# Optimization experiments

Hardware: AMD Instinct MI355X
Metric: run time of the kernel (lower is better)

## Reference

```python
import jax, jax.numpy as jnp
import numpy as np

B, S, D, H, F, L, V = 4, 512, 1024, 16, 4096, 6, 32000
HD = D // H
EPS = 1e-10


def layer_norm(x, g, b):
    m = x.mean(-1, keepdims=True)
    v = ((x - m) ** 2).mean(-1, keepdims=True)  # unbiased=False
    return g * (x - m) / jnp.sqrt(v + EPS) + b


def mha(q, k, v, wq, bq, wk, bk, wv, bv, wo, bo, mask):
    b_, s_, d_ = q.shape
    qh = (q @ wq + bq).reshape(b_, s_, H, HD).transpose(0, 2, 1, 3)  # [B,H,S,hd]
    kh = (k @ wk + bk).reshape(b_, s_, H, HD).transpose(0, 2, 1, 3)
    vh = (v @ wv + bv).reshape(b_, s_, H, HD).transpose(0, 2, 1, 3)
    score = jnp.einsum('bhqd,bhkd->bhqk', qh, kh) / jnp.sqrt(jnp.asarray(HD, q.dtype))
    score = jnp.where(mask == 0, jnp.asarray(-10000.0, q.dtype), score)
    attn = jax.nn.softmax(score, axis=-1)
    out = jnp.einsum('bhqk,bhkd->bhqd', attn, vh).transpose(0, 2, 1, 3).reshape(b_, s_, d_)
    return out @ wo + bo


def pos_encoding(seq, d):
    pos = jnp.arange(seq, dtype=jnp.float32)[:, None]
    i2 = jnp.arange(0, d, 2, dtype=jnp.float32)
    ang = pos / (10000.0 ** (i2 / d))
    enc = jnp.zeros((seq, d), jnp.float32)
    return enc.at[:, 0::2].set(jnp.sin(ang)).at[:, 1::2].set(jnp.cos(ang))


def setup_inputs() -> dict:
    key = jax.random.key(0)
    ks = iter(jax.random.split(key, 64))
    sd = 0.02
    inp = {
        'dec': jax.random.randint(next(ks), (B, S), 0, V),
        'enc': jax.random.normal(next(ks), (B, S, D), jnp.float32),
        't_mask': jnp.tril(jnp.ones((S, S), jnp.int32))[None, None],  # causal [1,1,S,S]
        's_mask': jnp.ones((1, 1, S, S), jnp.int32),
        'emb': (jax.random.normal(next(ks), (V, D), jnp.float32) * sd).at[1].set(0.0),  # padding_idx=1
    }
    for pre in ('sa', 'ca'):
        for nm in ('wq', 'wk', 'wv', 'wo'):
            inp[f'{pre}_{nm}'] = jax.random.normal(next(ks), (L, D, D), jnp.float32) * sd
            inp[f'{pre}_b{nm[1]}'] = jnp.zeros((L, D), jnp.float32)
    inp['ffn_w1'] = jax.random.normal(next(ks), (L, D, F), jnp.float32) * sd
    inp['ffn_b1'] = jnp.zeros((L, F), jnp.float32)
    inp['ffn_w2'] = jax.random.normal(next(ks), (L, F, D), jnp.float32) * sd
    inp['ffn_b2'] = jnp.zeros((L, D), jnp.float32)
    for i in (1, 2, 3):
        inp[f'ln{i}_g'] = jnp.ones((L, D), jnp.float32)
        inp[f'ln{i}_b'] = jnp.zeros((L, D), jnp.float32)
    inp['w_out'] = jax.random.normal(next(ks), (D, V), jnp.float32) * sd
    inp['b_out'] = jnp.zeros((V,), jnp.float32)
    return inp


def reference(dec, enc, t_mask, s_mask, emb,
              sa_wq, sa_bq, sa_wk, sa_bk, sa_wv, sa_bv, sa_wo, sa_bo,
              ca_wq, ca_bq, ca_wk, ca_bk, ca_wv, ca_bv, ca_wo, ca_bo,
              ffn_w1, ffn_b1, ffn_w2, ffn_b2,
              ln1_g, ln1_b, ln2_g, ln2_b, ln3_g, ln3_b, w_out, b_out):
    x = emb[dec] + pos_encoding(dec.shape[1], D)  # token + positional embedding
    for l in range(L):
        r = x
        a = mha(x, x, x, sa_wq[l], sa_bq[l], sa_wk[l], sa_bk[l], sa_wv[l], sa_bv[l], sa_wo[l], sa_bo[l], t_mask)
        x = layer_norm(a + r, ln1_g[l], ln1_b[l])
        r = x
        a = mha(x, enc, enc, ca_wq[l], ca_bq[l], ca_wk[l], ca_bk[l], ca_wv[l], ca_bv[l], ca_wo[l], ca_bo[l], s_mask)
        x = layer_norm(a + r, ln2_g[l], ln2_b[l])
        r = x
        f = jax.nn.relu(x @ ffn_w1[l] + ffn_b1[l]) @ ffn_w2[l] + ffn_b2[l]
        x = layer_norm(f + r, ln3_g[l], ln3_b[l])
    return x @ w_out + b_out  # [B,S,V] logits
```

## Files before the change

### kernel.cpp

```cpp
#include <hip/hip_runtime.h>
#include <hip/hip_bf16.h>
#include <math.h>

using bf16 = __hip_bfloat16;
typedef __attribute__((ext_vector_type(8))) short short8;
typedef __attribute__((ext_vector_type(4))) float f32x4;
typedef __attribute__((ext_vector_type(16))) float f32x16;

#define NTOKC 2048
#define DM 1024
#define SEQL 512
#define NHEADS 16
#define HDIM 64
#define FFDIM 4096
#define NLAYERS 6
#define VOCAB 32000

__device__ __forceinline__ void gld_lds16(const void* g, void* l) {
  __builtin_amdgcn_global_load_lds((__attribute__((address_space(1))) void*)g,
                                   (__attribute__((address_space(3))) void*)l, 16, 0, 0);
}

template<int BM, int BN>
__global__ __launch_bounds__(256, 3) void gemm_k(
    const bf16* __restrict__ A, const bf16* __restrict__ B, void* __restrict__ Cp,
    const float* __restrict__ bias, int K, int lda, int ldb, int ldc,
    long long sAb, long long sAh, long long sBb, long long sBh,
    long long sCb, long long sCh, int HH, int biasStride, float scale, int flags,
    int mTiles, const bf16* __restrict__ A2, int a2from)
{
  constexpr int WAM = BM/64;
  constexpr int WAN = 4/WAM;
  constexpr int WN  = BN/WAN;
  constexpr int FM  = 2;
  constexpr int FN  = WN/32;
  constexpr int NCA = (BM*64)/2048;
  constexpr int NCB = (BN*64)/2048;
  __shared__ __align__(16) bf16 As[BM*64];
  __shared__ __align__(16) bf16 Bs[BN*64];
  const int tid = threadIdx.x, w = tid>>6, l = tid&63;
  const int z = blockIdx.z, zb = z/HH, zh = z - zb*HH;
  const bf16* Abase = (zh >= a2from) ? A2 : A;
  const bf16* Ab = Abase + (size_t)zb*sAb + (size_t)zh*sAh;
  const bf16* Bb = B + (size_t)zb*sBb + (size_t)zh*sBh;

  const int nwg = gridDim.x;
  int o = blockIdx.x, idx = o;
  if ((nwg & 7) == 0) idx = (o & 7) * (nwg >> 3) + (o >> 3);
  const int mt = idx % mTiles, nt = idx / mTiles;
  const int m0 = mt*BM, n0 = nt*BN;

  const int wm = w / WAN, wn = w % WAN;
  const int lr = l & 31;
  const int lh = l >> 5;

  f32x16 acc[FM][FN];
  #pragma unroll
  for (int i=0;i<FM;i++)
    #pragma unroll
    for (int j=0;j<FN;j++)
      #pragma unroll
      for (int e=0;e<16;e++) acc[i][j][e] = 0.f;

  int rA[NCA], kA[NCA];
  #pragma unroll
  for (int c=0;c<NCA;c++){ int e=c*2048+tid*8; int r=e>>6, k=e&63; rA[c]=r; kA[c]=k ^ ((r&7)<<3); }
  int rB[NCB], kB[NCB];
  #pragma unroll
  for (int c=0;c<NCB;c++){ int e=c*2048+tid*8; int r=e>>6, k=e&63; rB[c]=r; kB[c]=k ^ ((r&7)<<3); }

  for (int kt=0; kt<K; kt+=64) {
    #pragma unroll
    for (int c=0;c<NCA;c++)
      gld_lds16(Ab + (size_t)(m0+rA[c])*lda + kt + kA[c], (char*)As + c*4096 + w*1024);
    #pragma unroll
    for (int c=0;c<NCB;c++)
      gld_lds16(Bb + (size_t)(n0+rB[c])*ldb + kt + kB[c], (char*)Bs + c*4096 + w*1024);
    __syncthreads();
    #pragma unroll
    for (int kq=0; kq<4; kq++) {
      const int kk = kq*16 + lh*8;
      short8 a_[FM], b_[FN];
      #pragma unroll
      for (int i=0;i<FM;i++) {
        const int row = wm*64 + i*32 + lr;
        a_[i] = *(const short8*)(As + row*64 + (kk ^ ((row&7)<<3)));
      }
      #pragma unroll
      for (int j=0;j<FN;j++) {
        const int row = wn*WN + j*32 + lr;
        b_[j] = *(const short8*)(Bs + row*64 + (kk ^ ((row&7)<<3)));
      }
      #pragma unroll
      for (int i=0;i<FM;i++)
        #pragma unroll
        for (int j=0;j<FN;j++)
          acc[i][j] = __builtin_amdgcn_mfma_f32_32x32x16_bf16(a_[i], b_[j], acc[i][j], 0,0,0);
    }
    __syncthreads();
  }

  const bool obf = flags & 1, orl = flags & 2;
  const size_t coff = (size_t)zb*sCb + (size_t)zh*sCh;
  const float* brow = bias ? (bias + (size_t)z*biasStride) : nullptr;
  #pragma unroll
  for (int i=0;i<FM;i++) {
    #pragma unroll
    for (int j=0;j<FN;j++) {
      const int col = n0 + wn*WN + j*32 + lr;
      const float bv = brow ? brow[col] : 0.f;
      const int row0 = m0 + wm*64 + i*32 + 4*lh;
      #pragma unroll
      for (int r=0;r<16;r++) {
        const int row = row0 + (r&3) + 8*(r>>2);
        float v = acc[i][j][r]*scale + bv;
        if (orl) v = fmaxf(v, 0.f);
        const size_t off = coff + (size_t)row*ldc + col;
        if (obf) ((bf16*)Cp)[off] = __float2bfloat16(v);
        else     ((float*)Cp)[off] = v;
      }
    }
  }
}

template<int CAUSAL>
__global__ __launch_bounds__(256, 4) void flash_k(
    const bf16* __restrict__ Qg, const bf16* __restrict__ Kg,
    const bf16* __restrict__ Vt, bf16* __restrict__ Og)
{
  constexpr int PADK = 72;
  __shared__ __align__(16) bf16 Ks[64*PADK];
  __shared__ __align__(16) bf16 Vs[64*PADK];
  __shared__ __align__(16) bf16 Ps[4*16*PADK];
  const int tid = threadIdx.x, w = tid>>6, l = tid&63;
  const int qt = blockIdx.x, bh = blockIdx.y;
  const int b = bh>>4, h = bh&15;
  const int q0 = qt*64;
  const int lr = l&15, lg = l>>4;

  const bf16* qrow = Qg + (size_t)(b*SEQL + q0 + w*16 + lr)*DM + h*HDIM + lg*8;
  short8 qf0 = *(const short8*)(qrow);
  short8 qf1 = *(const short8*)(qrow + 32);

  const f32x4 vzero = {0.f,0.f,0.f,0.f};
  f32x4 Oa[4];
  float mrow[4], lrow[4];
  #pragma unroll
  for (int j=0;j<4;j++) Oa[j] = vzero;
  #pragma unroll
  for (int r=0;r<4;r++){ mrow[r] = -INFINITY; lrow[r] = 0.f; }

  const int ntiles = CAUSAL ? (qt+1) : (SEQL/64);
  const int c0 = tid, c1 = tid + 256;
  const int r0_ = c0>>3, o0_ = (c0&7)*8, r1_ = c1>>3, o1_ = (c1&7)*8;

  short8 s0,s1,s2,s3;
  {
    s0 = *(const short8*)(Kg + (size_t)(b*SEQL + r0_)*DM + h*HDIM + o0_);
    s1 = *(const short8*)(Kg + (size_t)(b*SEQL + r1_)*DM + h*HDIM + o1_);
    s2 = *(const short8*)(Vt + ((size_t)bh*HDIM + r0_)*SEQL + o0_);
    s3 = *(const short8*)(Vt + ((size_t)bh*HDIM + r1_)*SEQL + o1_);
  }

  for (int t=0; t<ntiles; ++t) {
    __syncthreads();
    *(short8*)(Ks + r0_*PADK + o0_) = s0;
    *(short8*)(Ks + r1_*PADK + o1_) = s1;
    *(short8*)(Vs + r0_*PADK + o0_) = s2;
    *(short8*)(Vs + r1_*PADK + o1_) = s3;
    __syncthreads();
    if (t+1 < ntiles) {
      const int kv1 = (t+1)*64;
      s0 = *(const short8*)(Kg + (size_t)(b*SEQL + kv1 + r0_)*DM + h*HDIM + o0_);
      s1 = *(const short8*)(Kg + (size_t)(b*SEQL + kv1 + r1_)*DM + h*HDIM + o1_);
      s2 = *(const short8*)(Vt + ((size_t)bh*HDIM + r0_)*SEQL + kv1 + o0_);
      s3 = *(const short8*)(Vt + ((size_t)bh*HDIM + r1_)*SEQL + kv1 + o1_);
    }

    f32x4 sa[4];
    #pragma unroll
    for (int jg=0;jg<4;jg++) {
      short8 kb0 = *(const short8*)(Ks + (jg*16+lr)*PADK + lg*8);
      short8 kb1 = *(const short8*)(Ks + (jg*16+lr)*PADK + 32 + lg*8);
      sa[jg] = __builtin_amdgcn_mfma_f32_16x16x32_bf16(qf0, kb0, vzero, 0,0,0);
      sa[jg] = __builtin_amdgcn_mfma_f32_16x16x32_bf16(qf1, kb1, sa[jg], 0,0,0);
    }

    float pv[4][4];
    #pragma unroll
    for (int jg=0;jg<4;jg++)
      #pragma unroll
      for (int r=0;r<4;r++) {
        float sv = sa[jg][r]*0.125f;
        if (CAUSAL && t==ntiles-1) {
          if (jg*16+lr > w*16+lg*4+r) sv = -INFINITY;
        }
        pv[jg][r] = sv;
      }
    float tm[4], sf[4], rs[4];
    #pragma unroll
    for (int r=0;r<4;r++) {
      float mx = fmaxf(fmaxf(pv[0][r],pv[1][r]), fmaxf(pv[2][r],pv[3][r]));
      #pragma unroll
      for (int o=1;o<16;o<<=1) mx = fmaxf(mx, __shfl_xor(mx, o));
      tm[r] = fmaxf(mrow[r], mx);
      sf[r] = __expf(mrow[r]-tm[r]);
      mrow[r] = tm[r];
    }
    #pragma unroll
    for (int r=0;r<4;r++) {
      float acc = 0.f;
      #pragma unroll
      for (int jg=0;jg<4;jg++) { float e = __expf(pv[jg][r]-tm[r]); pv[jg][r]=e; acc += e; }
      #pragma unroll
      for (int o=1;o<16;o<<=1) acc += __shfl_xor(acc, o);
      rs[r] = acc;
      lrow[r] = lrow[r]*sf[r] + rs[r];
    }
    #pragma unroll
    for (int jg=0;jg<4;jg++)
      #pragma unroll
      for (int r=0;r<4;r++) Oa[jg][r] *= sf[r];

    bf16* pw = Ps + w*16*PADK;
    #pragma unroll
    for (int jg=0;jg<4;jg++)
      #pragma unroll
      for (int r=0;r<4;r++)
        pw[(lg*4+r)*PADK + jg*16+lr] = __float2bfloat16(pv[jg][r]);
    asm volatile("s_waitcnt lgkmcnt(0)" ::: "memory");
    __builtin_amdgcn_sched_barrier(0);
    short8 pa0 = *(const short8*)(pw + lr*PADK + lg*8);
    short8 pa1 = *(const short8*)(pw + lr*PADK + 32 + lg*8);
    #pragma unroll
    for (int jg=0;jg<4;jg++) {
      short8 vb0 = *(const short8*)(Vs + (jg*16+lr)*PADK + lg*8);
      short8 vb1 = *(const short8*)(Vs + (jg*16+lr)*PADK + 32 + lg*8);
      Oa[jg] = __builtin_amdgcn_mfma_f32_16x16x32_bf16(pa0, vb0, Oa[jg], 0,0,0);
      Oa[jg] = __builtin_amdgcn_mfma_f32_16x16x32_bf16(pa1, vb1, Oa[jg], 0,0,0);
    }
  }

  #pragma unroll
  for (int r=0;r<4;r++) {
    const float inv = 1.f/lrow[r];
    const size_t rb = (size_t)(b*SEQL + q0 + w*16 + lg*4 + r)*DM + h*HDIM;
    #pragma unroll
    for (int jg=0;jg<4;jg++)
      Og[rb + jg*16 + lr] = __float2bfloat16(Oa[jg][r]*inv);
  }
}

__global__ __launch_bounds__(256) void embed_k(const int* __restrict__ dec, const float* __restrict__ emb,
    float* __restrict__ x32, bf16* __restrict__ x16)
{
  const int idx = blockIdx.x*256 + threadIdx.x;
  const int d = idx & (DM-1), tok = idx >> 10, s = tok & (SEQL-1);
  const float e = emb[(size_t)dec[tok]*DM + d];
  const float den = powf(10000.f, (float)(d & ~1) * (1.f/(float)DM));
  const float ang = (float)s / den;
  const float pe = (d&1) ? cosf(ang) : sinf(ang);
  const float vv = e + pe;
  x32[idx] = vv; x16[idx] = __float2bfloat16(vv);
}

__global__ __launch_bounds__(256) void cvt_k(const float* __restrict__ in, bf16* __restrict__ out, int n){
  int i = blockIdx.x*256 + threadIdx.x;
  if (i < n) out[i] = __float2bfloat16(in[i]);
}

__global__ __launch_bounds__(256) void trans_k(const float* __restrict__ src, bf16* __restrict__ dst, int K, int N)
{
  __shared__ float t[32][33];
  const int n0 = blockIdx.x*32, k0 = blockIdx.y*32;
  const int tx = threadIdx.x&31, ty = threadIdx.x>>5;
  #pragma unroll
  for (int i=0;i<4;i++) t[ty+i*8][tx] = src[(size_t)(k0+ty+i*8)*N + n0+tx];
  __syncthreads();
  #pragma unroll
  for (int i=0;i<4;i++) dst[(size_t)(n0+ty+i*8)*K + k0+tx] = __float2bfloat16(t[tx][ty+i*8]);
}

struct TPack { const float* src[10]; bf16* dst[10]; int K[10]; int N[10]; int tile0[10]; };
__global__ __launch_bounds__(256) void transm_k(TPack p)
{
  __shared__ float t[32][33];
  const int id = blockIdx.x;
  int mi = 0;
  #pragma unroll
  for (int i=1;i<10;i++) if (id >= p.tile0[i]) mi = i;
  const float* src = p.src[mi]; bf16* dst = p.dst[mi];
  const int K = p.K[mi], N = p.N[mi];
  const int local = id - p.tile0[mi];
  const int ntn = N >> 5;
  const int nt = local % ntn, kt = local / ntn;
  const int n0 = nt*32, k0 = kt*32;
  const int tx = threadIdx.x&31, ty = threadIdx.x>>5;
  #pragma unroll
  for (int i=0;i<4;i++) t[ty+i*8][tx] = src[(size_t)(k0+ty+i*8)*N + n0+tx];
  __syncthreads();
  #pragma unroll
  for (int i=0;i<4;i++) dst[(size_t)(n0+ty+i*8)*K + k0+tx] = __float2bfloat16(t[tx][ty+i*8]);
}

struct BiasSrc { const float* s[6]; float* out; };
__global__ __launch_bounds__(256) void biaspack_k(BiasSrc p)
{
  const int i = blockIdx.x*256 + threadIdx.x;
  const int l = i / 6144, j = i - l*6144;
  const int m = j >> 10, c = j & 1023;
  p.out[i] = p.s[m][(size_t)l*DM + c];
}

__global__ __launch_bounds__(256) void vtrans_k(const bf16* __restrict__ v, bf16* __restrict__ vt)
{
  __shared__ bf16 t[32][33];
  const int bh = blockIdx.z, b = bh>>4, h = bh&15;
  const int s0 = blockIdx.x*32, d0 = blockIdx.y*32;
  const int tx = threadIdx.x&31, ty = threadIdx.x>>5;
  #pragma unroll
  for (int i=0;i<4;i++)
    t[ty+i*8][tx] = v[(size_t)(b*SEQL + s0+ty+i*8)*DM + h*HDIM + d0+tx];
  __syncthreads();
  #pragma unroll
  for (int i=0;i<4;i++)
    vt[((size_t)bh*HDIM + d0+ty+i*8)*SEQL + s0+tx] = t[tx][ty+i*8];
}

__global__ __launch_bounds__(256) void ln_k(const float* __restrict__ a, const float* __restrict__ r,
    const float* __restrict__ g, const float* __restrict__ be,
    float* __restrict__ y32, bf16* __restrict__ y16)
{
  const int row = blockIdx.x, t = threadIdx.x;
  const size_t base = (size_t)row*DM;
  float v[4]; float s = 0.f;
  #pragma unroll
  for (int i=0;i<4;i++){ int c=t+i*256; v[i] = a[base+c] + r[base+c]; s += v[i]; }
  __shared__ float red[8];
  #pragma unroll
  for (int o=32;o>0;o>>=1) s += __shfl_down(s,o);
  if ((t&63)==0) red[t>>6]=s;
  __syncthreads();
  const float mean = (red[0]+red[1]+red[2]+red[3]) * (1.f/1024.f);
  float vs = 0.f;
  #pragma unroll
  for (int i=0;i<4;i++){ float d=v[i]-mean; vs += d*d; }
  #pragma unroll
  for (int o=32;o>0;o>>=1) vs += __shfl_down(vs,o);
  if ((t&63)==0) red[4+(t>>6)]=vs;
  __syncthreads();
  const float var = (red[4]+red[5]+red[6]+red[7]) * (1.f/1024.f);
  const float rstd = rsqrtf(var + 1e-10f);
  #pragma unroll
  for (int i=0;i<4;i++){
    int c=t+i*256;
    float y = g[c]*(v[i]-mean)*rstd + be[c];
    y32[base+c] = y; y16[base+c] = __float2bfloat16(y);
  }
}

template<int CAUSAL>
static void run_attention(hipStream_t st, bf16* qkv, bf16* vt, bf16* ctx)
{
  vtrans_k<<<dim3(16,2,64),256,0,st>>>(qkv + (size_t)2*NTOKC*DM, vt);
  flash_k<CAUSAL><<<dim3(SEQL/64, 64),256,0,st>>>(qkv, qkv + (size_t)NTOKC*DM, vt, ctx);
}

extern "C" void kernel_launch(void* const* d_in, const int* in_sizes, int n_in,
                              void* d_out, int out_size, void* d_ws, size_t ws_size,
                              hipStream_t stream)
{
  (void)in_sizes; (void)n_in; (void)out_size;
  const int*   dec    = (const int*)  d_in[0];
  const float* enc    = (const float*)d_in[1];
  const float* emb    = (const float*)d_in[4];
  const float* sa_w[4] = { (const float*)d_in[5], (const float*)d_in[7], (const float*)d_in[9],  (const float*)d_in[11] };
  const float* sa_b[4] = { (const float*)d_in[6], (const float*)d_in[8], (const float*)d_in[10], (const float*)d_in[12] };
  const float* ca_w[4] = { (const float*)d_in[13], (const float*)d_in[15], (const float*)d_in[17], (const float*)d_in[19] };
  const float* ca_b[4] = { (const float*)d_in[14], (const float*)d_in[16], (const float*)d_in[18], (const float*)d_in[20] };
  const float* ffn_w1 = (const float*)d_in[21];
  const float* ffn_b1 = (const float*)d_in[22];
  const float* ffn_w2 = (const float*)d_in[23];
  const float* ffn_b2 = (const float*)d_in[24];
  const float* ln_g[3] = { (const float*)d_in[25], (const float*)d_in[27], (const float*)d_in[29] };
  const float* ln_b[3] = { (const float*)d_in[26], (const float*)d_in[28], (const float*)d_in[30] };
  const float* w_out  = (const float*)d_in[31];
  const float* b_out  = (const float*)d_in[32];
  float* out = (float*)d_out;

  char* p = (char*)d_ws;
  auto alloc = [&](size_t b)->char* { char* r=p; p += (b+255)&~(size_t)255; return r; };
  bf16* x16   = (bf16*)alloc((size_t)NTOKC*DM*2);
  bf16* enc16 = (bf16*)alloc((size_t)NTOKC*DM*2);
  bf16* qkv   = (bf16*)alloc((size_t)3*NTOKC*DM*2);
  bf16* ctx   = (bf16*)alloc((size_t)NTOKC*DM*2);
  bf16* vt    = (bf16*)alloc((size_t)64*HDIM*SEQL*2);
  bf16* mid   = (bf16*)alloc((size_t)NTOKC*FFDIM*2);
  bf16* wtA   = (bf16*)alloc((size_t)8*DM*DM*2);
  bf16* wtF1  = (bf16*)alloc((size_t)FFDIM*DM*2);
  bf16* wtF2  = (bf16*)alloc((size_t)DM*FFDIM*2);
  bf16* wtO   = (bf16*)alloc((size_t)VOCAB*DM*2);
  float* x32  = (float*)alloc((size_t)NTOKC*DM*4);
  float* aout = (float*)alloc((size_t)NTOKC*DM*4);
  float* biasAll = (float*)alloc((size_t)NLAYERS*6*DM*4);
  if ((size_t)(p - (char*)d_ws) > ws_size) return;

  embed_k<<<8192,256,0,stream>>>(dec, emb, x32, x16);
  cvt_k<<<8192,256,0,stream>>>(enc, enc16, NTOKC*DM);
  trans_k<<<dim3(VOCAB/32, DM/32),256,0,stream>>>(w_out, wtO, DM, VOCAB);
  {
    BiasSrc bs;
    bs.s[0]=sa_b[0]; bs.s[1]=sa_b[1]; bs.s[2]=sa_b[2];
    bs.s[3]=ca_b[0]; bs.s[4]=ca_b[1]; bs.s[5]=ca_b[2];
    bs.out = biasAll;
    biaspack_k<<<(NLAYERS*6*DM)/256,256,0,stream>>>(bs);
  }

  for (int l=0; l<NLAYERS; ++l) {
    {
      TPack tp;
      for (int i=0;i<4;i++){ tp.src[i]   = sa_w[i] + (size_t)l*DM*DM; tp.dst[i]   = wtA + (size_t)i*DM*DM;
                             tp.K[i]=DM; tp.N[i]=DM; tp.tile0[i]=i*1024; }
      for (int i=0;i<4;i++){ tp.src[4+i] = ca_w[i] + (size_t)l*DM*DM; tp.dst[4+i] = wtA + (size_t)(4+i)*DM*DM;
                             tp.K[4+i]=DM; tp.N[4+i]=DM; tp.tile0[4+i]=(4+i)*1024; }
      tp.src[8]=ffn_w1 + (size_t)l*DM*FFDIM; tp.dst[8]=wtF1; tp.K[8]=DM; tp.N[8]=FFDIM; tp.tile0[8]=8192;
      tp.src[9]=ffn_w2 + (size_t)l*FFDIM*DM; tp.dst[9]=wtF2; tp.K[9]=FFDIM; tp.N[9]=DM; tp.tile0[9]=12288;
      transm_k<<<16384,256,0,stream>>>(tp);
    }
    const float* biasL = biasAll + (size_t)l*6*DM;

    gemm_k<128,128><<<dim3(128,1,3),256,0,stream>>>(x16, wtA, qkv, biasL,
        DM, DM, DM, DM, 0,0, (long long)DM*DM,0, (long long)NTOKC*DM,0, 1, DM, 1.f, 1, 16, x16, 9);
    run_attention<1>(stream, qkv, vt, ctx);
    gemm_k<64,128><<<dim3(256,1,1),256,0,stream>>>(ctx, wtA + (size_t)3*DM*DM, aout, sa_b[3]+l*DM,
        DM, DM, DM, DM, 0,0,0,0,0,0, 1, 0, 1.f, 0, 32, ctx, 9);
    ln_k<<<2048,256,0,stream>>>(aout, x32, ln_g[0]+l*DM, ln_b[0]+l*DM, x32, x16);

    gemm_k<128,128><<<dim3(128,1,3),256,0,stream>>>(x16, wtA + (size_t)4*DM*DM, qkv, biasL + 3*DM,
        DM, DM, DM, DM, 0,0, 0,(long long)DM*DM, 0,(long long)NTOKC*DM, 3, DM, 1.f, 1, 16, enc16, 1);
    run_attention<0>(stream, qkv, vt, ctx);
    gemm_k<64,128><<<dim3(256,1,1),256,0,stream>>>(ctx, wtA + (size_t)7*DM*DM, aout, ca_b[3]+l*DM,
        DM, DM, DM, DM, 0,0,0,0,0,0, 1, 0, 1.f, 0, 32, ctx, 9);
    ln_k<<<2048,256,0,stream>>>(aout, x32, ln_g[1]+l*DM, ln_b[1]+l*DM, x32, x16);

    gemm_k<128,128><<<dim3(512,1,1),256,0,stream>>>(x16, wtF1, mid, ffn_b1 + (size_t)l*FFDIM,
        DM, DM, DM, FFDIM, 0,0,0,0,0,0, 1, 0, 1.f, 1|2, 16, x16, 9);
    gemm_k<64,128><<<dim3(256,1,1),256,0,stream>>>(mid, wtF2, aout, ffn_b2 + (size_t)l*DM,
        FFDIM, FFDIM, FFDIM, DM, 0,0,0,0,0,0, 1, 0, 1.f, 0, 32, mid, 9);
    ln_k<<<2048,256,0,stream>>>(aout, x32, ln_g[2]+l*DM, ln_b[2]+l*DM, x32, x16);
  }

  gemm_k<128,128><<<dim3(4000,1,1),256,0,stream>>>(x16, wtO, out, b_out,
      DM, DM, DM, VOCAB, 0,0,0,0,0,0, 1, 0, 1.f, 0, 16, x16, 9);
}
```

Measured before the change: 1.752 ms.

## Fuse V transpose into QKV GEMM epilogue and split-K output projections

The QKV projection GEMM now writes the V slice directly in transposed per-head layout through an LDS staging tile, which removes the separate vtrans kernel launches. The output-projection and FFN2 GEMMs now use a 2-way split-K across blockIdx.z, doubling the grid from 256 blocks to fill more CUs. The two partial sums plus the bias are added inside the layernorm kernel. This costs an extra fp32 partial buffer written and read per layer, and a more complex GEMM epilogue.

```diff
diff --git a/kernel.cpp b/kernel.cpp
--- a/kernel.cpp
+++ b/kernel.cpp
@@ -27,7 +27,7 @@
     const float* __restrict__ bias, int K, int lda, int ldb, int ldc,
     long long sAb, long long sAh, long long sBb, long long sBh,
     long long sCb, long long sCh, int HH, int biasStride, float scale, int flags,
-    int mTiles, const bf16* __restrict__ A2, int a2from)
+    int mTiles, const bf16* __restrict__ A2, int a2from, bf16* __restrict__ VT)
 {
   constexpr int WAM = BM/64;
   constexpr int WAN = 4/WAM;
@@ -36,8 +36,9 @@
   constexpr int FN  = WN/32;
   constexpr int NCA = (BM*64)/2048;
   constexpr int NCB = (BN*64)/2048;
-  __shared__ __align__(16) bf16 As[BM*64];
-  __shared__ __align__(16) bf16 Bs[BN*64];
+  __shared__ __align__(16) bf16 Smem[BM*64 + BN*64];
+  bf16* As = Smem;
+  bf16* Bs = Smem + BM*64;
   const int tid = threadIdx.x, w = tid>>6, l = tid&63;
   const int z = blockIdx.z, zb = z/HH, zh = z - zb*HH;
   const bf16* Abase = (zh >= a2from) ? A2 : A;
@@ -100,9 +101,45 @@
     __syncthreads();
   }
 
+  const float* brow = bias ? (bias + (size_t)z*biasStride) : nullptr;
+
+  if (BM==128 && BN==128 && (flags & 4) && zh == 2) {
+    bf16* T = Smem + w*4096;
+    #pragma unroll
+    for (int i=0;i<FM;i++) {
+      #pragma unroll
+      for (int j=0;j<FN;j++) {
+        const int cl = j*32 + lr;
+        const float bv = brow ? brow[n0 + wn*WN + cl] : 0.f;
+        #pragma unroll
+        for (int r=0;r<16;r++) {
+          const int sl = i*32 + 4*lh + (r&3) + 8*(r>>2);
+          T[sl*64 + (cl ^ (sl & 63))] = __float2bfloat16(acc[i][j][r]*scale + bv);
+        }
+      }
+    }
+    asm volatile("s_waitcnt lgkmcnt(0)" ::: "memory");
+    __builtin_amdgcn_sched_barrier(0);
+    const int token0 = m0 + wm*64;
+    const int bb = token0 >> 9, sbase = token0 & 511;
+    const int h = (n0 + wn*WN) >> 6;
+    #pragma unroll
+    for (int it=0; it<8; ++it) {
+      const int crow = it*8 + (l>>3);
+      const int s0 = (l&7)*8;
+      short8 v8;
+      #pragma unroll
+      for (int k=0;k<8;k++) {
+        const int s = s0 + k;
+        v8[k] = *(const short*)&T[s*64 + (crow ^ (s & 63))];
+      }
+      *(short8*)(VT + (((size_t)(bb*16 + h)*64 + crow)*512 + sbase + s0)) = v8;
+    }
+    return;
+  }
+
   const bool obf = flags & 1, orl = flags & 2;
   const size_t coff = (size_t)zb*sCb + (size_t)zh*sCh;
-  const float* brow = bias ? (bias + (size_t)z*biasStride) : nullptr;
   #pragma unroll
   for (int i=0;i<FM;i++) {
     #pragma unroll
@@ -312,22 +349,8 @@
   p.out[i] = p.s[m][(size_t)l*DM + c];
 }
 
-__global__ __launch_bounds__(256) void vtrans_k(const bf16* __restrict__ v, bf16* __restrict__ vt)
-{
-  __shared__ bf16 t[32][33];
-  const int bh = blockIdx.z, b = bh>>4, h = bh&15;
-  const int s0 = blockIdx.x*32, d0 = blockIdx.y*32;
-  const int tx = threadIdx.x&31, ty = threadIdx.x>>5;
-  #pragma unroll
-  for (int i=0;i<4;i++)
-    t[ty+i*8][tx] = v[(size_t)(b*SEQL + s0+ty+i*8)*DM + h*HDIM + d0+tx];
-  __syncthreads();
-  #pragma unroll
-  for (int i=0;i<4;i++)
-    vt[((size_t)bh*HDIM + d0+ty+i*8)*SEQL + s0+tx] = t[tx][ty+i*8];
-}
-
-__global__ __launch_bounds__(256) void ln_k(const float* __restrict__ a, const float* __restrict__ r,
+__global__ __launch_bounds__(256) void ln_k(const float* __restrict__ a, const float* __restrict__ a2,
+    const float* __restrict__ gb, const float* __restrict__ r,
     const float* __restrict__ g, const float* __restrict__ be,
     float* __restrict__ y32, bf16* __restrict__ y16)
 {
@@ -335,7 +358,7 @@
   const size_t base = (size_t)row*DM;
   float v[4]; float s = 0.f;
   #pragma unroll
-  for (int i=0;i<4;i++){ int c=t+i*256; v[i] = a[base+c] + r[base+c]; s += v[i]; }
+  for (int i=0;i<4;i++){ int c=t+i*256; v[i] = a[base+c] + a2[base+c] + gb[c] + r[base+c]; s += v[i]; }
   __shared__ float red[8];
   #pragma unroll
   for (int o=32;o>0;o>>=1) s += __shfl_down(s,o);
@@ -357,13 +380,6 @@
     float y = g[c]*(v[i]-mean)*rstd + be[c];
     y32[base+c] = y; y16[base+c] = __float2bfloat16(y);
   }
-}
-
-template<int CAUSAL>
-static void run_attention(hipStream_t st, bf16* qkv, bf16* vt, bf16* ctx)
-{
-  vtrans_k<<<dim3(16,2,64),256,0,st>>>(qkv + (size_t)2*NTOKC*DM, vt);
-  flash_k<CAUSAL><<<dim3(SEQL/64, 64),256,0,st>>>(qkv, qkv + (size_t)NTOKC*DM, vt, ctx);
 }
 
 extern "C" void kernel_launch(void* const* d_in, const int* in_sizes, int n_in,
@@ -401,9 +417,10 @@
   bf16* wtF2  = (bf16*)alloc((size_t)DM*FFDIM*2);
   bf16* wtO   = (bf16*)alloc((size_t)VOCAB*DM*2);
   float* x32  = (float*)alloc((size_t)NTOKC*DM*4);
-  float* aout = (float*)alloc((size_t)NTOKC*DM*4);
+  float* aout = (float*)alloc((size_t)2*NTOKC*DM*4);
   float* biasAll = (float*)alloc((size_t)NLAYERS*6*DM*4);
   if ((size_t)(p - (char*)d_ws) > ws_size) return;
+  float* aout2 = aout + (size_t)NTOKC*DM;
 
   embed_k<<<8192,256,0,stream>>>(dec, emb, x32, x16);
   cvt_k<<<8192,256,0,stream>>>(enc, enc16, NTOKC*DM);
@@ -430,26 +447,26 @@
     const float* biasL = biasAll + (size_t)l*6*DM;
 
     gemm_k<128,128><<<dim3(128,1,3),256,0,stream>>>(x16, wtA, qkv, biasL,
-        DM, DM, DM, DM, 0,0, (long long)DM*DM,0, (long long)NTOKC*DM,0, 1, DM, 1.f, 1, 16, x16, 9);
-    run_attention<1>(stream, qkv, vt, ctx);
-    gemm_k<64,128><<<dim3(256,1,1),256,0,stream>>>(ctx, wtA + (size_t)3*DM*DM, aout, sa_b[3]+l*DM,
-        DM, DM, DM, DM, 0,0,0,0,0,0, 1, 0, 1.f, 0, 32, ctx, 9);
-    ln_k<<<2048,256,0,stream>>>(aout, x32, ln_g[0]+l*DM, ln_b[0]+l*DM, x32, x16);
+        DM, DM, DM, DM, 0,0, 0,(long long)DM*DM, 0,(long long)NTOKC*DM, 3, DM, 1.f, 1|4, 16, x16, 9, vt);
+    flash_k<1><<<dim3(SEQL/64, 64),256,0,stream>>>(qkv, qkv + (size_t)NTOKC*DM, vt, ctx);
+    gemm_k<64,128><<<dim3(256,1,2),256,0,stream>>>(ctx, wtA + (size_t)3*DM*DM, aout, nullptr,
+        512, DM, DM, DM, 0,512, 0,512, 0,(long long)NTOKC*DM, 2, 0, 1.f, 0, 32, ctx, 9, nullptr);
+    ln_k<<<2048,256,0,stream>>>(aout, aout2, sa_b[3]+l*DM, x32, ln_g[0]+l*DM, ln_b[0]+l*DM, x32, x16);
 
     gemm_k<128,128><<<dim3(128,1,3),256,0,stream>>>(x16, wtA + (size_t)4*DM*DM, qkv, biasL + 3*DM,
-        DM, DM, DM, DM, 0,0, 0,(long long)DM*DM, 0,(long long)NTOKC*DM, 3, DM, 1.f, 1, 16, enc16, 1);
-    run_attention<0>(stream, qkv, vt, ctx);
-    gemm_k<64,128><<<dim3(256,1,1),256,0,stream>>>(ctx, wtA + (size_t)7*DM*DM, aout, ca_b[3]+l*DM,
-        DM, DM, DM, DM, 0,0,0,0,0,0, 1, 0, 1.f, 0, 32, ctx, 9);
-    ln_k<<<2048,256,0,stream>>>(aout, x32, ln_g[1]+l*DM, ln_b[1]+l*DM, x32, x16);
+        DM, DM, DM, DM, 0,0, 0,(long long)DM*DM, 0,(long long)NTOKC*DM, 3, DM, 1.f, 1|4, 16, enc16, 1, vt);
+    flash_k<0><<<dim3(SEQL/64, 64),256,0,stream>>>(qkv, qkv + (size_t)NTOKC*DM, vt, ctx);
+    gemm_k<64,128><<<dim3(256,1,2),256,0,stream>>>(ctx, wtA + (size_t)7*DM*DM, aout, nullptr,
+        512, DM, DM, DM, 0,512, 0,512, 0,(long long)NTOKC*DM, 2, 0, 1.f, 0, 32, ctx, 9, nullptr);
+    ln_k<<<2048,256,0,stream>>>(aout, aout2, ca_b[3]+l*DM, x32, ln_g[1]+l*DM, ln_b[1]+l*DM, x32, x16);
 
     gemm_k<128,128><<<dim3(512,1,1),256,0,stream>>>(x16, wtF1, mid, ffn_b1 + (size_t)l*FFDIM,
-        DM, DM, DM, FFDIM, 0,0,0,0,0,0, 1, 0, 1.f, 1|2, 16, x16, 9);
-    gemm_k<64,128><<<dim3(256,1,1),256,0,stream>>>(mid, wtF2, aout, ffn_b2 + (size_t)l*DM,
-        FFDIM, FFDIM, FFDIM, DM, 0,0,0,0,0,0, 1, 0, 1.f, 0, 32, mid, 9);
-    ln_k<<<2048,256,0,stream>>>(aout, x32, ln_g[2]+l*DM, ln_b[2]+l*DM, x32, x16);
+        DM, DM, DM, FFDIM, 0,0,0,0,0,0, 1, 0, 1.f, 1|2, 16, x16, 9, nullptr);
+    gemm_k<64,128><<<dim3(256,1,2),256,0,stream>>>(mid, wtF2, aout, nullptr,
+        2048, FFDIM, FFDIM, DM, 0,2048, 0,2048, 0,(long long)NTOKC*DM, 2, 0, 1.f, 0, 32, mid, 9, nullptr);
+    ln_k<<<2048,256,0,stream>>>(aout, aout2, ffn_b2 + (size_t)l*DM, x32, ln_g[2]+l*DM, ln_b[2]+l*DM, x32, x16);
   }
 
   gemm_k<128,128><<<dim3(4000,1,1),256,0,stream>>>(x16, wtO, out, b_out,
-      DM, DM, DM, VOCAB, 0,0,0,0,0,0, 1, 0, 1.f, 0, 16, x16, 9);
-}
+      DM, DM, DM, VOCAB, 0,0,0,0,0,0, 1, 0, 1.f, 0, 16, x16, 9, nullptr);
+}
```

Result: faster. 1.519 ms (-13.3%).
